# Kernel optimization log

Hardware: AMD Instinct MI355X
Metric: run time of the kernel (lower is better)

## Reference

```python
import jax, jax.numpy as jnp
import numpy as np

DIM = 512
NUM_HEADS = 8
HEAD_DIM = DIM // NUM_HEADS
SR = 2
LN_EPS = 1e-5


def setup_inputs() -> dict:
    key = jax.random.key(0)
    ks = jax.random.split(key, 12)
    B, H, W = 8, 32, 32
    N = H * W
    s = 0.02
    return {
        "x": jax.random.normal(ks[0], (B, N, DIM), jnp.float32),
        "H": H,
        "W": W,
        # weights stored as [in, out] (torch Linear applies x @ W.T + b)
        "q_w": jax.random.normal(ks[1], (DIM, DIM), jnp.float32) * s,
        "q_b": jnp.zeros((DIM,), jnp.float32),
        "kv_w": jax.random.normal(ks[2], (DIM, 2 * DIM), jnp.float32) * s,
        "kv_b": jnp.zeros((2 * DIM,), jnp.float32),
        "sr_w": jax.random.normal(ks[3], (DIM, DIM, SR, SR), jnp.float32) * s,  # OIHW
        "sr_b": jnp.zeros((DIM,), jnp.float32),
        "ln_g": jnp.ones((DIM,), jnp.float32),
        "ln_b": jnp.zeros((DIM,), jnp.float32),
        "proj_w": jax.random.normal(ks[4], (DIM, DIM), jnp.float32) * s,
        "proj_b": jnp.zeros((DIM,), jnp.float32),
    }


def reference(x, H, W, q_w, q_b, kv_w, kv_b, sr_w, sr_b, ln_g, ln_b, proj_w, proj_b):
    B, N, C = x.shape
    hd = HEAD_DIM
    scale = hd ** -0.5

    # q: [B, nh, N, hd]
    q = (x @ q_w + q_b).reshape(B, N, NUM_HEADS, hd).transpose(0, 2, 1, 3)

    # spatial reduction conv (stride=kernel=SR) + LayerNorm
    x2d = x.transpose(0, 2, 1).reshape(B, C, H, W)
    x2d = jax.lax.conv_general_dilated(
        x2d, sr_w, window_strides=(SR, SR), padding="VALID",
        dimension_numbers=("NCHW", "OIHW", "NCHW")) + sr_b[None, :, None, None]
    Nk = x2d.shape[2] * x2d.shape[3]
    x_kv = x2d.reshape(B, C, Nk).transpose(0, 2, 1)  # [B, Nk, C]
    mu = x_kv.mean(-1, keepdims=True)
    var = ((x_kv - mu) ** 2).mean(-1, keepdims=True)
    x_kv = (x_kv - mu) * jax.lax.rsqrt(var + LN_EPS) * ln_g + ln_b

    kv = x_kv @ kv_w + kv_b  # [B, Nk, 2C]
    k, v = kv[..., :C], kv[..., C:]
    # Faithful to torch: reshape folds C/hd into kv-sequence axis -> M = Nk*num_heads,
    # shared (broadcast) across all query heads.
    M = Nk * NUM_HEADS
    k = k.reshape(B, M, hd)
    v = v.reshape(B, M, hd)

    attn = jnp.einsum("bhnd,bmd->bhnm", q, k) * scale  # [B, nh, N, M]
    attn = jax.nn.softmax(attn, axis=-1)
    out = jnp.einsum("bhnm,bmd->bhnd", attn, v)  # [B, nh, N, hd]
    out = out.transpose(0, 2, 1, 3).reshape(B, N, C)
    return out @ proj_w + proj_b
```

## Files before the change

### kernel.cpp

```cpp
#include <hip/hip_runtime.h>
#include <hip/hip_bf16.h>
#include <stdint.h>

typedef __attribute__((ext_vector_type(8))) short short8;
typedef __attribute__((ext_vector_type(4))) float f32x4;

#define MFMA(A, B, C) __builtin_amdgcn_mfma_f32_16x16x32_bf16(A, B, C, 0, 0, 0)

__device__ inline uint32_t bfrne(float f) {
  uint32_t u = __float_as_uint(f);
  return (u + 0x7FFFu + ((u >> 16) & 1u)) >> 16;
}

__device__ inline uint32_t pkrne(float a, float b) {
  union { __hip_bfloat162 v; uint32_t u; } c;
  c.v.x = __float2bfloat16(a);
  c.v.y = __float2bfloat16(b);
  return c.u;
}

__device__ inline float fexp2(float x) { return __builtin_amdgcn_exp2f(x); }

__device__ inline void gload16(const short* g, short* l) {
  __builtin_amdgcn_global_load_lds(
      (const __attribute__((address_space(1))) void*)g,
      (__attribute__((address_space(3))) void*)l, 16, 0, 0);
}

__global__ __launch_bounds__(256) void prep_all_kernel(
    const float* __restrict__ sr_w, const float* __restrict__ kv_w,
    const float* __restrict__ q_w, const float* __restrict__ proj_w,
    const float* __restrict__ x,
    short* __restrict__ WcThi, short* __restrict__ kvThi,
    short* __restrict__ qThi, short* __restrict__ pThi,
    short* __restrict__ xhi) {
  __shared__ float tile[32][33];
  const int blk = blockIdx.x;
  if (blk < 4096) {
    int t = blk * 256 + threadIdx.x;
    int kk = t & 2047, o = t >> 11;
    float v = sr_w[(size_t)o * 2048 + ((kk & 511) << 2) + (kk >> 9)];
    WcThi[t] = (short)bfrne(v);
    return;
  }
  if (blk >= 5120) {
    int t = (blk - 5120) * 256 + threadIdx.x;
    float4 v0 = *(const float4*)&x[(size_t)t * 8];
    float4 v1 = *(const float4*)&x[(size_t)t * 8 + 4];
    uint4 pk;
    pk.x = pkrne(v0.x, v0.y);
    pk.y = pkrne(v0.z, v0.w);
    pk.z = pkrne(v1.x, v1.y);
    pk.w = pkrne(v1.z, v1.w);
    *(uint4*)&xhi[(size_t)t * 8] = pk;
    return;
  }
  const float* in; short* ohi; int N, bx, by;
  if (blk < 4608) {
    in = kv_w; ohi = kvThi; N = 1024;
    int i = blk - 4096; bx = i & 31; by = i >> 5;
  } else if (blk < 4864) {
    in = q_w; ohi = qThi; N = 512;
    int i = blk - 4608; bx = i & 15; by = i >> 4;
  } else {
    in = proj_w; ohi = pThi; N = 512;
    int i = blk - 4864; bx = i & 15; by = i >> 4;
  }
  const int K = 512;
  const int tx = threadIdx.x & 31, ty = threadIdx.x >> 5;
#pragma unroll
  for (int i = 0; i < 4; ++i)
    tile[ty + i * 8][tx] = in[(size_t)(by * 32 + ty + i * 8) * N + bx * 32 + tx];
  __syncthreads();
#pragma unroll
  for (int i = 0; i < 4; ++i) {
    int n = bx * 32 + ty + i * 8;
    float v = tile[tx][ty + i * 8];
    ohi[(size_t)n * K + by * 32 + tx] = (short)bfrne(v);
  }
}

__global__ __launch_bounds__(256) void ln_kernel(
    const float* __restrict__ X, const float* __restrict__ g,
    const float* __restrict__ bta, short* __restrict__ hi) {
  const int row = blockIdx.x, t = threadIdx.x;
  size_t idx = (size_t)row * 512 + t * 2;
  const size_t PS = (size_t)2048 * 512;
  float2 a0 = *(const float2*)&X[idx];
  float2 a1 = *(const float2*)&X[idx + PS];
  float2 a2 = *(const float2*)&X[idx + 2 * PS];
  float2 a3 = *(const float2*)&X[idx + 3 * PS];
  float x0 = a0.x + a1.x + a2.x + a3.x;
  float x1 = a0.y + a1.y + a2.y + a3.y;
  float s = x0 + x1, sq = x0 * x0 + x1 * x1;
#pragma unroll
  for (int off = 1; off < 64; off <<= 1) {
    s += __shfl_xor(s, off);
    sq += __shfl_xor(sq, off);
  }
  __shared__ float rs[4], rq[4];
  int wid = t >> 6;
  if ((t & 63) == 0) { rs[wid] = s; rq[wid] = sq; }
  __syncthreads();
  s = rs[0] + rs[1] + rs[2] + rs[3];
  sq = rq[0] + rq[1] + rq[2] + rq[3];
  float mu = s * (1.f / 512), var = sq * (1.f / 512) - mu * mu;
  float inv = rsqrtf(var + 1e-5f);
  float2 gg = *(const float2*)&g[t * 2], bb = *(const float2*)&bta[t * 2];
  float o0 = (x0 - mu) * inv * gg.x + bb.x;
  float o1 = (x1 - mu) * inv * gg.y + bb.y;
  *(uint32_t*)&hi[idx] = pkrne(o0, o1);
}

template <bool GATHER, int OMODE>
__device__ __forceinline__ void gemm_body(
    short* ldsraw,
    const short* __restrict__ Ahi, const short* __restrict__ BThi,
    const float* __restrict__ bias, float* __restrict__ C,
    short* __restrict__ Chi, short* __restrict__ Vfo, float oscale,
    int M, int N, int lda, int ldb, int klen,
    int bxx, int byy, int bzz) {
  typedef short (*ldsA_t)[64][8];
  typedef short (*ldsB_t)[128][8];
  ldsA_t ldsA = (ldsA_t)ldsraw;
  ldsB_t ldsB = (ldsB_t)(ldsraw + 8 * 64 * 8);
  const int tid = threadIdx.x, lane = tid & 63, wave = tid >> 6;
  const int g = lane >> 4, qi = lane & 15;
  const int row0 = bxx * 64, col0 = byy * 128;
  const int kz = bzz * klen;
  float* Cz = C + (size_t)bzz * M * N;
  const bool dobias = (bzz == 0);
  f32x4 acc[4][2] = {};

  for (int k0 = kz; k0 < kz + klen; k0 += 64) {
    __syncthreads();
#pragma unroll
    for (int r = 0; r < 2; ++r) {
      int c = tid + r * 256;
      int arow = c & 63, akg = c >> 6;
      size_t ao;
      if (GATHER) {
        int row = row0 + arow;
        int bi = row >> 8, p = row & 255;
        int col = k0 + akg * 8;
        int seg = col >> 9, cc = col & 511;
        int n = (2 * (p >> 4) + (seg >> 1)) * 32 + 2 * (p & 15) + (seg & 1);
        ao = ((size_t)bi * 1024 + n) * 512 + cc;
      } else {
        ao = (size_t)(row0 + arow) * lda + k0 + akg * 8;
      }
      gload16(&Ahi[ao], &ldsA[akg][arow][0]);
    }
#pragma unroll
    for (int r = 0; r < 4; ++r) {
      int c = tid + r * 256;
      int bcol = c & 127, bkg = c >> 7;
      size_t bo = (size_t)(col0 + bcol) * ldb + k0 + bkg * 8;
      gload16(&BThi[bo], &ldsB[bkg][bcol][0]);
    }
    __syncthreads();
#pragma unroll
    for (int kk = 0; kk < 2; ++kk) {
      const int kg = kk * 4 + g;
      short8 ah[4], bh[2];
#pragma unroll
      for (int i = 0; i < 4; ++i)
        ah[i] = *(const short8*)&ldsA[kg][i * 16 + qi][0];
#pragma unroll
      for (int j = 0; j < 2; ++j)
        bh[j] = *(const short8*)&ldsB[kg][wave * 32 + j * 16 + qi][0];
#pragma unroll
      for (int i = 0; i < 4; ++i)
#pragma unroll
        for (int j = 0; j < 2; ++j)
          acc[i][j] = MFMA(ah[i], bh[j], acc[i][j]);
    }
  }
#pragma unroll
  for (int i = 0; i < 4; ++i)
#pragma unroll
    for (int j = 0; j < 2; ++j) {
      int colb = col0 + wave * 32 + j * 16 + qi;
      float bs = dobias ? bias[colb] : 0.f;
#pragma unroll
      for (int r = 0; r < 4; ++r) {
        int row = row0 + i * 16 + g * 4 + r;
        if (OMODE == 0) {
          Cz[(size_t)row * N + colb] = acc[i][j][r] + bs;
        } else if (OMODE == 1) {
          Chi[(size_t)row * N + colb] = (short)bfrne((acc[i][j][r] + bs) * oscale);
        } else {
          uint32_t hv = bfrne(acc[i][j][r] + bs);
          int bb2 = row >> 8, p = row & 255;
          if (colb < 512) {
            int m = p * 8 + (colb >> 6), d = colb & 63;
            size_t t = ((((size_t)(bb2 * 32 + (m >> 6)) * 8 +
                          ((m >> 4) & 3) * 2 + (d >> 5)) * 64) +
                        ((d >> 3) & 3) * 16 + (m & 15)) * 8 + (d & 7);
            Chi[t] = (short)hv;
          } else {
            int c2 = colb - 512;
            int m = p * 8 + (c2 >> 6), d = c2 & 63;
            size_t t = ((((size_t)(bb2 * 32 + (m >> 6)) * 8 +
                          ((m >> 5) & 1) * 4 + (d >> 4)) * 64) +
                        ((m >> 3) & 3) * 16 + (d & 15)) * 8 + (m & 7);
            Vfo[t] = (short)hv;
          }
        }
      }
    }
}

template <bool GATHER, int OMODE>
__global__ __launch_bounds__(256) void gemm_1p(
    const short* __restrict__ Ahi, const short* __restrict__ BThi,
    const float* __restrict__ bias, float* __restrict__ C,
    short* __restrict__ Chi, short* __restrict__ Vfo, float oscale,
    int M, int N, int lda, int ldb, int klen) {
  __shared__ short lds[12288];
  gemm_body<GATHER, OMODE>(lds, Ahi, BThi, bias, C, Chi, Vfo, oscale,
                           M, N, lda, ldb, klen,
                           blockIdx.x, blockIdx.y, blockIdx.z);
}

__global__ __launch_bounds__(256) void conv_q_kernel(
    const short* __restrict__ xhi, const short* __restrict__ WcThi,
    const float* __restrict__ sr_b, float* __restrict__ Cbuf,
    const short* __restrict__ qThi, const float* __restrict__ q_b,
    short* __restrict__ Qhi, float qscale) {
  __shared__ short lds[12288];
  const int blk = blockIdx.x;
  if (blk < 512) {
    int bx = blk & 31, by = (blk >> 5) & 3, bz = blk >> 7;
    gemm_body<true, 0>(lds, xhi, WcThi, sr_b, Cbuf, nullptr, nullptr, 1.f,
                       2048, 512, 512, 2048, 512, bx, by, bz);
  } else {
    int i = blk - 512;
    int bx = i & 127, by = i >> 7;
    gemm_body<false, 1>(lds, xhi, qThi, q_b, nullptr, Qhi, nullptr, qscale,
                        8192, 512, 512, 512, 512, bx, by, 0);
  }
}

__device__ __forceinline__ void ld8(short8 (&dst)[8], const short* base) {
#pragma unroll
  for (int i = 0; i < 8; ++i)
    dst[i] = *(const short8*)&base[(size_t)i * 512];
}

__device__ __forceinline__ void qk_tile(f32x4 (&s)[2][4], const short8 (&kr)[8],
                                        const short8 (&qh)[2][2]) {
  const f32x4 z = {0.f, 0.f, 0.f, 0.f};
  __builtin_amdgcn_s_setprio(1);
#pragma unroll
  for (int mf = 0; mf < 4; ++mf)
#pragma unroll
    for (int qc = 0; qc < 2; ++qc) {
      s[qc][mf] = MFMA(kr[mf * 2 + 0], qh[qc][0], z);
      s[qc][mf] = MFMA(kr[mf * 2 + 1], qh[qc][1], s[qc][mf]);
    }
  __builtin_amdgcn_s_setprio(0);
}

__device__ __forceinline__ void pack_tile(const f32x4 (&s)[2][4], short* Psw,
                                          int g, int qi, int swz) {
#pragma unroll
  for (int qc = 0; qc < 2; ++qc)
#pragma unroll
    for (int mf = 0; mf < 4; ++mf) {
      uint32_t u0 = __float_as_uint(fexp2(s[qc][mf][0]));
      uint32_t u1 = __float_as_uint(fexp2(s[qc][mf][1]));
      uint32_t u2 = __float_as_uint(fexp2(s[qc][mf][2]));
      uint32_t u3 = __float_as_uint(fexp2(s[qc][mf][3]));
      uint2 hp;
      hp.x = (u0 >> 16) | (u1 & 0xffff0000u);
      hp.y = (u2 >> 16) | (u3 & 0xffff0000u);
      int uw = ((mf * 4 + g) ^ swz) << 2;
      *(uint2*)&Psw[qc * 1024 + qi * 64 + uw] = hp;
    }
}

__device__ __forceinline__ void pv_tile(const short8 (&vr)[8], short* Psw,
                                        f32x4 (&lacc)[2], f32x4 (&oacc)[2][4],
                                        int g, int qi, int swz) {
  const short8 ones = {(short)0x3F80, (short)0x3F80, (short)0x3F80, (short)0x3F80,
                       (short)0x3F80, (short)0x3F80, (short)0x3F80, (short)0x3F80};
#pragma unroll
  for (int qc = 0; qc < 2; ++qc)
#pragma unroll
    for (int ks2 = 0; ks2 < 2; ++ks2) {
      int ur = ((ks2 * 8 + g * 2) ^ swz) << 2;
      short8 pa = *(const short8*)&Psw[qc * 1024 + qi * 64 + ur];
      __builtin_amdgcn_s_setprio(1);
      lacc[qc] = MFMA(ones, pa, lacc[qc]);
#pragma unroll
      for (int df = 0; df < 4; ++df)
        oacc[qc][df] = MFMA(vr[ks2 * 4 + df], pa, oacc[qc][df]);
      __builtin_amdgcn_s_setprio(0);
    }
}

__global__ __launch_bounds__(256, 2) void attn_kernel(
    const short* __restrict__ Qhi, const short* __restrict__ Kf,
    const short* __restrict__ Vf, short* __restrict__ Ohi) {
  __shared__ short Ps[4][2][1024];
  const int tid = threadIdx.x, lane = tid & 63, wave = tid >> 6;
  const int g = lane >> 4, qi = lane & 15;
  const int h = blockIdx.y, b = blockIdx.z;
  const int n0 = blockIdx.x * 128 + wave * 32;
  const int swz = (qi & 7) << 1;
  short* Psw = &Ps[wave][0][0];

  short8 qh[2][2];
#pragma unroll
  for (int qc = 0; qc < 2; ++qc) {
    const size_t qrow = ((size_t)b * 1024 + n0 + qc * 16 + qi) * 512 + h * 64;
#pragma unroll
    for (int ks = 0; ks < 2; ++ks)
      qh[qc][ks] = *(const short8*)&Qhi[qrow + (ks * 4 + g) * 8];
  }
  f32x4 lacc[2] = {};
  f32x4 oacc[2][4] = {};
  const short* Kb = Kf + (size_t)b * 131072 + lane * 8;
  const short* Vb = Vf + (size_t)b * 131072 + lane * 8;

  short8 kA[8], kB[8], vr[8];
  f32x4 sA[2][4], sB[2][4];
  ld8(kA, Kb);
  ld8(kB, Kb + 4096);
  qk_tile(sA, kA, qh);
  for (int t = 0; t < 32; t += 2) {
    const short* tK = Kb + (size_t)t * 4096;
    const short* tV = Vb + (size_t)t * 4096;
    ld8(vr, tV);
    if (t < 30) ld8(kA, tK + 8192);
    pack_tile(sA, Psw, g, qi, swz);
    qk_tile(sB, kB, qh);
    pv_tile(vr, Psw, lacc, oacc, g, qi, swz);
    ld8(vr, tV + 4096);
    if (t < 30) ld8(kB, tK + 12288);
    pack_tile(sB, Psw, g, qi, swz);
    if (t < 30) qk_tile(sA, kA, qh);
    pv_tile(vr, Psw, lacc, oacc, g, qi, swz);
  }
#pragma unroll
  for (int qc = 0; qc < 2; ++qc) {
    float linv = 1.f / lacc[qc][0];
    size_t obase = ((size_t)b * 1024 + n0 + qc * 16 + qi) * 512 + h * 64;
#pragma unroll
    for (int df = 0; df < 4; ++df) {
      float o0 = oacc[qc][df][0] * linv, o1 = oacc[qc][df][1] * linv;
      float o2 = oacc[qc][df][2] * linv, o3 = oacc[qc][df][3] * linv;
      uint2 hp;
      hp.x = pkrne(o0, o1);
      hp.y = pkrne(o2, o3);
      *(uint2*)&Ohi[obase + df * 16 + g * 4] = hp;
    }
  }
}

extern "C" void kernel_launch(void* const* d_in, const int* in_sizes, int n_in,
                              void* d_out, int out_size, void* d_ws, size_t ws_size,
                              hipStream_t stream) {
  const float* x      = (const float*)d_in[0];
  const float* q_w    = (const float*)d_in[3];
  const float* q_b    = (const float*)d_in[4];
  const float* kv_w   = (const float*)d_in[5];
  const float* kv_b   = (const float*)d_in[6];
  const float* sr_w   = (const float*)d_in[7];
  const float* sr_b   = (const float*)d_in[8];
  const float* ln_g   = (const float*)d_in[9];
  const float* ln_b   = (const float*)d_in[10];
  const float* proj_w = (const float*)d_in[11];
  const float* proj_b = (const float*)d_in[12];

  char* W = (char*)d_ws;
  const size_t MB = 1024 * 1024;
  short* xhi   = (short*)(W);
  short* WcThi = (short*)(W + 16 * MB);
  float* Cbuf  = (float*)(W + 20 * MB);
  short* LNhi  = (short*)(W + 36 * MB);
  short* kvThi = (short*)(W + 40 * MB);
  short* qThi  = (short*)(W + 42 * MB);
  short* pThi  = (short*)(W + 43 * MB);
  short* Qhi   = (short*)(W + 44 * MB);
  short* Kf    = (short*)(W + 20 * MB);
  short* Vf    = (short*)(W + 22 * MB);
  short* Ohi   = (short*)(W);

  prep_all_kernel<<<7168, 256, 0, stream>>>(
      sr_w, kv_w, q_w, proj_w, x, WcThi, kvThi, qThi, pThi, xhi);
  conv_q_kernel<<<1024, 256, 0, stream>>>(
      xhi, WcThi, sr_b, Cbuf, qThi, q_b, Qhi, 0.125f * 1.44269504f);
  ln_kernel<<<2048, 256, 0, stream>>>(Cbuf, ln_g, ln_b, LNhi);
  gemm_1p<false, 2><<<dim3(32, 8, 1), 256, 0, stream>>>(
      LNhi, kvThi, kv_b, nullptr, Kf, Vf, 1.f, 2048, 1024, 512, 512, 512);
  attn_kernel<<<dim3(8, 8, 8), 256, 0, stream>>>(Qhi, Kf, Vf, Ohi);
  gemm_1p<false, 0><<<dim3(128, 4, 1), 256, 0, stream>>>(
      Ohi, pThi, proj_b, (float*)d_out, nullptr, nullptr, 1.f,
      8192, 512, 512, 512, 512);
}
```

Baseline: 118.7 us.

## Halve attention rows per wave and double the attention grid

Each wave in the attention kernel now handles 16 query rows instead of 32, and the grid grows from 512 to 1024 blocks. The skewed QK/PV software pipeline is replaced by a simpler sequential per-tile routine that runs QK, exp/pack and PV back to back, with K/V loads prefetched one tile ahead. The aim is more blocks and fewer registers for better occupancy and load balance across CUs. The cost is that each K/V tile is loaded and reused for half as many query rows, doubling K/V global traffic, and QK MFMAs no longer overlap with the exp/pack work.

```diff
diff --git a/kernel.cpp b/kernel.cpp
--- a/kernel.cpp
+++ b/kernel.cpp
@@ -248,114 +248,90 @@
     dst[i] = *(const short8*)&base[(size_t)i * 512];
 }
 
-__device__ __forceinline__ void qk_tile(f32x4 (&s)[2][4], const short8 (&kr)[8],
-                                        const short8 (&qh)[2][2]) {
+__device__ __forceinline__ void attn_tile16(
+    const short8 (&kr)[8], const short8 (&vr)[8], const short8 (&qh)[2],
+    f32x4& lacc, f32x4 (&oacc)[4], short* Psw, int g, int qi, int swz) {
+  const short8 ones = {(short)0x3F80, (short)0x3F80, (short)0x3F80, (short)0x3F80,
+                       (short)0x3F80, (short)0x3F80, (short)0x3F80, (short)0x3F80};
+  f32x4 s[4];
   const f32x4 z = {0.f, 0.f, 0.f, 0.f};
   __builtin_amdgcn_s_setprio(1);
 #pragma unroll
-  for (int mf = 0; mf < 4; ++mf)
-#pragma unroll
-    for (int qc = 0; qc < 2; ++qc) {
-      s[qc][mf] = MFMA(kr[mf * 2 + 0], qh[qc][0], z);
-      s[qc][mf] = MFMA(kr[mf * 2 + 1], qh[qc][1], s[qc][mf]);
-    }
+  for (int mf = 0; mf < 4; ++mf) {
+    s[mf] = MFMA(kr[mf * 2 + 0], qh[0], z);
+    s[mf] = MFMA(kr[mf * 2 + 1], qh[1], s[mf]);
+  }
   __builtin_amdgcn_s_setprio(0);
-}
-
-__device__ __forceinline__ void pack_tile(const f32x4 (&s)[2][4], short* Psw,
-                                          int g, int qi, int swz) {
-#pragma unroll
-  for (int qc = 0; qc < 2; ++qc)
-#pragma unroll
-    for (int mf = 0; mf < 4; ++mf) {
-      uint32_t u0 = __float_as_uint(fexp2(s[qc][mf][0]));
-      uint32_t u1 = __float_as_uint(fexp2(s[qc][mf][1]));
-      uint32_t u2 = __float_as_uint(fexp2(s[qc][mf][2]));
-      uint32_t u3 = __float_as_uint(fexp2(s[qc][mf][3]));
-      uint2 hp;
-      hp.x = (u0 >> 16) | (u1 & 0xffff0000u);
-      hp.y = (u2 >> 16) | (u3 & 0xffff0000u);
-      int uw = ((mf * 4 + g) ^ swz) << 2;
-      *(uint2*)&Psw[qc * 1024 + qi * 64 + uw] = hp;
-    }
-}
-
-__device__ __forceinline__ void pv_tile(const short8 (&vr)[8], short* Psw,
-                                        f32x4 (&lacc)[2], f32x4 (&oacc)[2][4],
-                                        int g, int qi, int swz) {
-  const short8 ones = {(short)0x3F80, (short)0x3F80, (short)0x3F80, (short)0x3F80,
-                       (short)0x3F80, (short)0x3F80, (short)0x3F80, (short)0x3F80};
-#pragma unroll
-  for (int qc = 0; qc < 2; ++qc)
-#pragma unroll
-    for (int ks2 = 0; ks2 < 2; ++ks2) {
-      int ur = ((ks2 * 8 + g * 2) ^ swz) << 2;
-      short8 pa = *(const short8*)&Psw[qc * 1024 + qi * 64 + ur];
-      __builtin_amdgcn_s_setprio(1);
-      lacc[qc] = MFMA(ones, pa, lacc[qc]);
-#pragma unroll
-      for (int df = 0; df < 4; ++df)
-        oacc[qc][df] = MFMA(vr[ks2 * 4 + df], pa, oacc[qc][df]);
-      __builtin_amdgcn_s_setprio(0);
-    }
+#pragma unroll
+  for (int mf = 0; mf < 4; ++mf) {
+    uint32_t u0 = __float_as_uint(fexp2(s[mf][0]));
+    uint32_t u1 = __float_as_uint(fexp2(s[mf][1]));
+    uint32_t u2 = __float_as_uint(fexp2(s[mf][2]));
+    uint32_t u3 = __float_as_uint(fexp2(s[mf][3]));
+    uint2 hp;
+    hp.x = (u0 >> 16) | (u1 & 0xffff0000u);
+    hp.y = (u2 >> 16) | (u3 & 0xffff0000u);
+    int uw = ((mf * 4 + g) ^ swz) << 2;
+    *(uint2*)&Psw[qi * 64 + uw] = hp;
+  }
+#pragma unroll
+  for (int ks2 = 0; ks2 < 2; ++ks2) {
+    int ur = ((ks2 * 8 + g * 2) ^ swz) << 2;
+    short8 pa = *(const short8*)&Psw[qi * 64 + ur];
+    __builtin_amdgcn_s_setprio(1);
+    lacc = MFMA(ones, pa, lacc);
+#pragma unroll
+    for (int df = 0; df < 4; ++df)
+      oacc[df] = MFMA(vr[ks2 * 4 + df], pa, oacc[df]);
+    __builtin_amdgcn_s_setprio(0);
+  }
 }
 
 __global__ __launch_bounds__(256, 2) void attn_kernel(
     const short* __restrict__ Qhi, const short* __restrict__ Kf,
     const short* __restrict__ Vf, short* __restrict__ Ohi) {
-  __shared__ short Ps[4][2][1024];
+  __shared__ short Ps[4][1024];
   const int tid = threadIdx.x, lane = tid & 63, wave = tid >> 6;
   const int g = lane >> 4, qi = lane & 15;
   const int h = blockIdx.y, b = blockIdx.z;
-  const int n0 = blockIdx.x * 128 + wave * 32;
+  const int n0 = blockIdx.x * 64 + wave * 16;
   const int swz = (qi & 7) << 1;
-  short* Psw = &Ps[wave][0][0];
-
-  short8 qh[2][2];
-#pragma unroll
-  for (int qc = 0; qc < 2; ++qc) {
-    const size_t qrow = ((size_t)b * 1024 + n0 + qc * 16 + qi) * 512 + h * 64;
+  short* Psw = &Ps[wave][0];
+
+  short8 qh[2];
+  {
+    const size_t qrow = ((size_t)b * 1024 + n0 + qi) * 512 + h * 64;
 #pragma unroll
     for (int ks = 0; ks < 2; ++ks)
-      qh[qc][ks] = *(const short8*)&Qhi[qrow + (ks * 4 + g) * 8];
-  }
-  f32x4 lacc[2] = {};
-  f32x4 oacc[2][4] = {};
+      qh[ks] = *(const short8*)&Qhi[qrow + (ks * 4 + g) * 8];
+  }
+  f32x4 lacc = {};
+  f32x4 oacc[4] = {};
   const short* Kb = Kf + (size_t)b * 131072 + lane * 8;
   const short* Vb = Vf + (size_t)b * 131072 + lane * 8;
 
   short8 kA[8], kB[8], vr[8];
-  f32x4 sA[2][4], sB[2][4];
   ld8(kA, Kb);
-  ld8(kB, Kb + 4096);
-  qk_tile(sA, kA, qh);
-  for (int t = 0; t < 32; t += 2) {
-    const short* tK = Kb + (size_t)t * 4096;
-    const short* tV = Vb + (size_t)t * 4096;
+  for (int it = 0; it < 16; ++it) {
+    const short* tK = Kb + (size_t)it * 8192;
+    const short* tV = Vb + (size_t)it * 8192;
+    ld8(kB, tK + 4096);
     ld8(vr, tV);
-    if (t < 30) ld8(kA, tK + 8192);
-    pack_tile(sA, Psw, g, qi, swz);
-    qk_tile(sB, kB, qh);
-    pv_tile(vr, Psw, lacc, oacc, g, qi, swz);
+    attn_tile16(kA, vr, qh, lacc, oacc, Psw, g, qi, swz);
+    if (it < 15) ld8(kA, tK + 8192);
     ld8(vr, tV + 4096);
-    if (t < 30) ld8(kB, tK + 12288);
-    pack_tile(sB, Psw, g, qi, swz);
-    if (t < 30) qk_tile(sA, kA, qh);
-    pv_tile(vr, Psw, lacc, oacc, g, qi, swz);
-  }
-#pragma unroll
-  for (int qc = 0; qc < 2; ++qc) {
-    float linv = 1.f / lacc[qc][0];
-    size_t obase = ((size_t)b * 1024 + n0 + qc * 16 + qi) * 512 + h * 64;
-#pragma unroll
-    for (int df = 0; df < 4; ++df) {
-      float o0 = oacc[qc][df][0] * linv, o1 = oacc[qc][df][1] * linv;
-      float o2 = oacc[qc][df][2] * linv, o3 = oacc[qc][df][3] * linv;
-      uint2 hp;
-      hp.x = pkrne(o0, o1);
-      hp.y = pkrne(o2, o3);
-      *(uint2*)&Ohi[obase + df * 16 + g * 4] = hp;
-    }
+    attn_tile16(kB, vr, qh, lacc, oacc, Psw, g, qi, swz);
+  }
+  float linv = 1.f / lacc[0];
+  size_t obase = ((size_t)b * 1024 + n0 + qi) * 512 + h * 64;
+#pragma unroll
+  for (int df = 0; df < 4; ++df) {
+    float o0 = oacc[df][0] * linv, o1 = oacc[df][1] * linv;
+    float o2 = oacc[df][2] * linv, o3 = oacc[df][3] * linv;
+    uint2 hp;
+    hp.x = pkrne(o0, o1);
+    hp.y = pkrne(o2, o3);
+    *(uint2*)&Ohi[obase + df * 16 + g * 4] = hp;
   }
 }
 
@@ -395,7 +371,7 @@
   ln_kernel<<<2048, 256, 0, stream>>>(Cbuf, ln_g, ln_b, LNhi);
   gemm_1p<false, 2><<<dim3(32, 8, 1), 256, 0, stream>>>(
       LNhi, kvThi, kv_b, nullptr, Kf, Vf, 1.f, 2048, 1024, 512, 512, 512);
-  attn_kernel<<<dim3(8, 8, 8), 256, 0, stream>>>(Qhi, Kf, Vf, Ohi);
+  attn_kernel<<<dim3(16, 8, 8), 256, 0, stream>>>(Qhi, Kf, Vf, Ohi);
   gemm_1p<false, 0><<<dim3(128, 4, 1), 256, 0, stream>>>(
       Ohi, pThi, proj_b, (float*)d_out, nullptr, nullptr, 1.f,
       8192, 512, 512, 512, 512);
```

Result: slower. 147.7 us (+24.4%).
